# Kernel optimization log

Hardware: AMD Instinct MI355X
Metric: run time of the kernel (lower is better)

## Reference

```python
import jax, jax.numpy as jnp
import numpy as np

WINDOW_SIZE = 11
SIGMA = 1.5
C1 = 0.01 ** 2
C2 = 0.03 ** 2


def _make_window(channel, dtype=jnp.float32):
    # Faithful to torch `gaussian`: center at window_size/2 (= 5.5 for ws=11)
    x = np.arange(WINDOW_SIZE, dtype=np.float64)
    g = np.exp(-((x - WINDOW_SIZE / 2) ** 2) / (2.0 * SIGMA ** 2))
    g = (g / g.sum()).astype(np.float32)
    w2d = np.outer(g, g)  # (ws, ws)
    w = np.broadcast_to(w2d, (channel, 1, WINDOW_SIZE, WINDOW_SIZE)).copy()
    return jnp.asarray(w, dtype=dtype)


def _dwconv(x, w, channel):
    pad = WINDOW_SIZE // 2
    return jax.lax.conv_general_dilated(
        x, w,
        window_strides=(1, 1),
        padding=[(pad, pad), (pad, pad)],
        dimension_numbers=("NCHW", "OIHW", "NCHW"),
        feature_group_count=channel,
    )


def setup_inputs() -> dict:
    key = jax.random.key(0)
    k1, k2 = jax.random.split(key)
    B, C, H, W = 16, 3, 512, 512
    img1 = jax.random.uniform(k1, (B, C, H, W), dtype=jnp.float32)
    img2 = jax.random.uniform(k2, (B, C, H, W), dtype=jnp.float32)
    return {"img1": img1, "img2": img2}


def reference(img1, img2):
    channel = img1.shape[1]
    window = _make_window(channel, img1.dtype)

    mu1 = _dwconv(img1, window, channel)
    mu2 = _dwconv(img2, window, channel)
    mu1_sq = mu1 * mu1
    mu2_sq = mu2 * mu2
    mu1_mu2 = mu1 * mu2

    sigma1_sq = _dwconv(img1 * img1, window, channel) - mu1_sq
    sigma2_sq = _dwconv(img2 * img2, window, channel) - mu2_sq
    sigma12 = _dwconv(img1 * img2, window, channel) - mu1_mu2

    numerator = (2 * mu1_mu2 + C1) * (2 * sigma12 + C2)
    denominator = (mu1_sq + mu2_sq + C1) * (sigma1_sq + sigma2_sq + C2)
    ssim_map = numerator / denominator
    return jnp.mean(ssim_map)  # size_average=True
```

## Files before the change

kernel.cpp:

```cpp
#include <hip/hip_runtime.h>
#include <cmath>


#define IMG_H 512
#define IMG_W 512
#define STRIPE 32
#define NSTR (IMG_H / STRIPE)
#define NPLANES 48
#define NBLOCKS (NPLANES * NSTR)
#define SSIM_C1 (0.01f * 0.01f)
#define SSIM_C2 (0.03f * 0.03f)

struct W11 { float w[11]; };

__launch_bounds__(512, 2)
__global__ void ssim_main(const float* __restrict__ img1,
                          const float* __restrict__ img2,
                          float* __restrict__ blockSums, W11 wv) {
    __shared__ float2 tb[2][528];
    __shared__ float red[8];

    const int x = threadIdx.x;
    const int bid = blockIdx.x;
    const int plane = bid >> 4;
    const int stripe = bid & (NSTR - 1);
    const int y0 = stripe * STRIPE;
    const size_t base = (size_t)plane * (IMG_H * IMG_W);

    if (x < 10) {
        const int col = (x < 5) ? x : (x + 512);
        tb[0][col] = make_float2(0.f, 0.f);
        tb[1][col] = make_float2(0.f, 0.f);
    }

    float rA[11], rB[11], rS[11], rP[11];
    float acc = 0.f;

    float pa = 0.f, pb = 0.f;
    {
        const int r0 = y0 - 5;
        if (r0 >= 0) {
            pa = img1[base + (size_t)r0 * IMG_W + x];
            pb = img2[base + (size_t)r0 * IMG_W + x];
        }
    }

    int buf = 0;
#pragma unroll 1
    for (int c = 0; c < 4; ++c) {
#pragma unroll
        for (int j = 0; j < 11; ++j) {
            const int i = c * 11 + j;
            if (i < 42) {
                tb[buf][x + 5] = make_float2(pa, pb);
                pa = 0.f; pb = 0.f;
                const int rn = y0 - 4 + i;
                if (i + 1 < 42 && rn >= 0 && rn < IMG_H) {
                    pa = img1[base + (size_t)rn * IMG_W + x];
                    pb = img2[base + (size_t)rn * IMG_W + x];
                }
                __syncthreads();
                float h0 = 0.f, h1 = 0.f, h2 = 0.f, h3 = 0.f;
#pragma unroll
                for (int k = 0; k < 11; ++k) {
                    const float2 t = tb[buf][x + k];
                    const float w = wv.w[k];
                    const float sq = fmaf(t.y, t.y, t.x * t.x);
                    const float pr = t.x * t.y;
                    h0 = fmaf(w, t.x, h0);
                    h1 = fmaf(w, t.y, h1);
                    h2 = fmaf(w, sq, h2);
                    h3 = fmaf(w, pr, h3);
                }
                rA[j] = h0; rB[j] = h1; rS[j] = h2; rP[j] = h3;

                if (i >= 10) {
                    float vA = 0.f, vB = 0.f, vS = 0.f, vP = 0.f;
#pragma unroll
                    for (int k = 0; k < 11; ++k) {
                        const int s = (j + 1 + k) % 11;
                        const float w = wv.w[k];
                        vA = fmaf(w, rA[s], vA);
                        vB = fmaf(w, rB[s], vB);
                        vS = fmaf(w, rS[s], vS);
                        vP = fmaf(w, rP[s], vP);
                    }
                    const float mu11 = vA * vA;
                    const float mu22 = vB * vB;
                    const float mu12 = vA * vB;
                    const float num = fmaf(2.f, mu12, SSIM_C1) *
                                      fmaf(2.f, vP - mu12, SSIM_C2);
                    const float d1  = mu11 + mu22;
                    const float den = (d1 + SSIM_C1) * ((vS - d1) + SSIM_C2);
                    acc = fmaf(num, __builtin_amdgcn_rcpf(den), acc);
                }
                buf ^= 1;
            }
        }
    }

#pragma unroll
    for (int off = 32; off >= 1; off >>= 1)
        acc += __shfl_down(acc, off, 64);
    const int wave = x >> 6, lane = x & 63;
    if (lane == 0) red[wave] = acc;
    __syncthreads();
    if (x == 0) {
        float s = 0.f;
#pragma unroll
        for (int k = 0; k < 8; ++k) s += red[k];
        blockSums[bid] = s;
    }
}

__global__ void ssim_reduce(const float* __restrict__ bs,
                            float* __restrict__ out) {
    __shared__ double red[4];
    const int t = threadIdx.x;
    double a = 0.0;
    for (int idx = t; idx < NBLOCKS; idx += 256) a += (double)bs[idx];
#pragma unroll
    for (int off = 32; off >= 1; off >>= 1)
        a += __shfl_down(a, off, 64);
    const int wave = t >> 6, lane = t & 63;
    if (lane == 0) red[wave] = a;
    __syncthreads();
    if (t == 0) {
        const double s = red[0] + red[1] + red[2] + red[3];
        out[0] = (float)(s / (double)((double)NPLANES * IMG_H * IMG_W));
    }
}

extern "C" void kernel_launch(void* const* d_in, const int* in_sizes, int n_in,
                              void* d_out, int out_size, void* d_ws, size_t ws_size,
                              hipStream_t stream) {
    const float* img1 = (const float*)d_in[0];
    const float* img2 = (const float*)d_in[1];
    float* out = (float*)d_out;
    float* bs = (float*)d_ws;

    W11 wv;
    double g[11], s = 0.0;
    for (int i = 0; i < 11; ++i) {
        const double d = (double)i - 5.5;
        g[i] = exp(-(d * d) / (2.0 * 1.5 * 1.5));
        s += g[i];
    }
    for (int i = 0; i < 11; ++i) wv.w[i] = (float)(g[i] / s);

    ssim_main<<<NBLOCKS, 512, 0, stream>>>(img1, img2, bs, wv);
    ssim_reduce<<<1, 256, 0, stream>>>(bs, out);
}
```

Measured before the change: 150.8 us.

## Compute two output columns per thread with vectorized loads and 256-thread blocks

Each thread now handles two adjacent columns. Global loads become float2, and shared-memory reads become float4, so a 12-wide window is loaded once and reused for both columns' horizontal sums. The block size halves to 256 threads and the launch bounds change to 256,3. This cuts shared-memory traffic and instruction overhead per output pixel, but it doubles the per-thread register arrays (8x11 floats), which risks spills or lower occupancy.

Result: no change. 153.3 us (+1.6%).

```diff
diff --git a/kernel.cpp b/kernel.cpp
--- a/kernel.cpp
+++ b/kernel.cpp
@@ -13,35 +13,36 @@
 
 struct W11 { float w[11]; };
 
-__launch_bounds__(512, 2)
+__launch_bounds__(256, 3)
 __global__ void ssim_main(const float* __restrict__ img1,
                           const float* __restrict__ img2,
                           float* __restrict__ blockSums, W11 wv) {
-    __shared__ float2 tb[2][528];
-    __shared__ float red[8];
+    __shared__ __align__(16) float2 tb[2][528];
+    __shared__ float red[4];
 
-    const int x = threadIdx.x;
+    const int t = threadIdx.x;
     const int bid = blockIdx.x;
     const int plane = bid >> 4;
     const int stripe = bid & (NSTR - 1);
     const int y0 = stripe * STRIPE;
     const size_t base = (size_t)plane * (IMG_H * IMG_W);
 
-    if (x < 10) {
-        const int col = (x < 5) ? x : (x + 512);
+    if (t < 10) {
+        const int col = (t < 5) ? t : (t + 512);
         tb[0][col] = make_float2(0.f, 0.f);
         tb[1][col] = make_float2(0.f, 0.f);
     }
 
-    float rA[11], rB[11], rS[11], rP[11];
+    float rA0[11], rB0[11], rS0[11], rP0[11];
+    float rA1[11], rB1[11], rS1[11], rP1[11];
     float acc = 0.f;
 
-    float pa = 0.f, pb = 0.f;
+    float2 pa = make_float2(0.f, 0.f), pb = make_float2(0.f, 0.f);
     {
         const int r0 = y0 - 5;
         if (r0 >= 0) {
-            pa = img1[base + (size_t)r0 * IMG_W + x];
-            pb = img2[base + (size_t)r0 * IMG_W + x];
+            pa = *(const float2*)(img1 + base + (size_t)r0 * IMG_W + 2 * t);
+            pb = *(const float2*)(img2 + base + (size_t)r0 * IMG_W + 2 * t);
         }
     }
 
@@ -52,47 +53,84 @@
         for (int j = 0; j < 11; ++j) {
             const int i = c * 11 + j;
             if (i < 42) {
-                tb[buf][x + 5] = make_float2(pa, pb);
-                pa = 0.f; pb = 0.f;
+                tb[buf][2 * t + 5] = make_float2(pa.x, pb.x);
+                tb[buf][2 * t + 6] = make_float2(pa.y, pb.y);
+                pa = make_float2(0.f, 0.f); pb = make_float2(0.f, 0.f);
                 const int rn = y0 - 4 + i;
                 if (i + 1 < 42 && rn >= 0 && rn < IMG_H) {
-                    pa = img1[base + (size_t)rn * IMG_W + x];
-                    pb = img2[base + (size_t)rn * IMG_W + x];
+                    pa = *(const float2*)(img1 + base + (size_t)rn * IMG_W + 2 * t);
+                    pb = *(const float2*)(img2 + base + (size_t)rn * IMG_W + 2 * t);
                 }
                 __syncthreads();
-                float h0 = 0.f, h1 = 0.f, h2 = 0.f, h3 = 0.f;
+
+                float ta[12], tbv[12];
 #pragma unroll
-                for (int k = 0; k < 11; ++k) {
-                    const float2 t = tb[buf][x + k];
-                    const float w = wv.w[k];
-                    const float sq = fmaf(t.y, t.y, t.x * t.x);
-                    const float pr = t.x * t.y;
-                    h0 = fmaf(w, t.x, h0);
-                    h1 = fmaf(w, t.y, h1);
-                    h2 = fmaf(w, sq, h2);
-                    h3 = fmaf(w, pr, h3);
+                for (int k = 0; k < 6; ++k) {
+                    const float4 q = *(const float4*)(&tb[buf][2 * t + 2 * k]);
+                    ta[2 * k]     = q.x; tbv[2 * k]     = q.y;
+                    ta[2 * k + 1] = q.z; tbv[2 * k + 1] = q.w;
                 }
-                rA[j] = h0; rB[j] = h1; rS[j] = h2; rP[j] = h3;
+                float hA0 = 0.f, hB0 = 0.f, hS0 = 0.f, hP0 = 0.f;
+                float hA1 = 0.f, hB1 = 0.f, hS1 = 0.f, hP1 = 0.f;
+#pragma unroll
+                for (int m = 0; m < 12; ++m) {
+                    const float a = ta[m], b = tbv[m];
+                    const float sq = fmaf(b, b, a * a);
+                    const float pr = a * b;
+                    if (m <= 10) {
+                        const float w = wv.w[m];
+                        hA0 = fmaf(w, a, hA0);
+                        hB0 = fmaf(w, b, hB0);
+                        hS0 = fmaf(w, sq, hS0);
+                        hP0 = fmaf(w, pr, hP0);
+                    }
+                    if (m >= 1) {
+                        const float w = wv.w[m - 1];
+                        hA1 = fmaf(w, a, hA1);
+                        hB1 = fmaf(w, b, hB1);
+                        hS1 = fmaf(w, sq, hS1);
+                        hP1 = fmaf(w, pr, hP1);
+                    }
+                }
+                rA0[j] = hA0; rB0[j] = hB0; rS0[j] = hS0; rP0[j] = hP0;
+                rA1[j] = hA1; rB1[j] = hB1; rS1[j] = hS1; rP1[j] = hP1;
 
                 if (i >= 10) {
-                    float vA = 0.f, vB = 0.f, vS = 0.f, vP = 0.f;
+                    float vA0 = 0.f, vB0 = 0.f, vS0 = 0.f, vP0 = 0.f;
+                    float vA1 = 0.f, vB1 = 0.f, vS1 = 0.f, vP1 = 0.f;
 #pragma unroll
                     for (int k = 0; k < 11; ++k) {
                         const int s = (j + 1 + k) % 11;
                         const float w = wv.w[k];
-                        vA = fmaf(w, rA[s], vA);
-                        vB = fmaf(w, rB[s], vB);
-                        vS = fmaf(w, rS[s], vS);
-                        vP = fmaf(w, rP[s], vP);
+                        vA0 = fmaf(w, rA0[s], vA0);
+                        vB0 = fmaf(w, rB0[s], vB0);
+                        vS0 = fmaf(w, rS0[s], vS0);
+                        vP0 = fmaf(w, rP0[s], vP0);
+                        vA1 = fmaf(w, rA1[s], vA1);
+                        vB1 = fmaf(w, rB1[s], vB1);
+                        vS1 = fmaf(w, rS1[s], vS1);
+                        vP1 = fmaf(w, rP1[s], vP1);
                     }
-                    const float mu11 = vA * vA;
-                    const float mu22 = vB * vB;
-                    const float mu12 = vA * vB;
-                    const float num = fmaf(2.f, mu12, SSIM_C1) *
-                                      fmaf(2.f, vP - mu12, SSIM_C2);
-                    const float d1  = mu11 + mu22;
-                    const float den = (d1 + SSIM_C1) * ((vS - d1) + SSIM_C2);
-                    acc = fmaf(num, __builtin_amdgcn_rcpf(den), acc);
+                    {
+                        const float mu11 = vA0 * vA0;
+                        const float mu22 = vB0 * vB0;
+                        const float mu12 = vA0 * vB0;
+                        const float num = fmaf(2.f, mu12, SSIM_C1) *
+                                          fmaf(2.f, vP0 - mu12, SSIM_C2);
+                        const float d1  = mu11 + mu22;
+                        const float den = (d1 + SSIM_C1) * ((vS0 - d1) + SSIM_C2);
+                        acc = fmaf(num, __builtin_amdgcn_rcpf(den), acc);
+                    }
+                    {
+                        const float mu11 = vA1 * vA1;
+                        const float mu22 = vB1 * vB1;
+                        const float mu12 = vA1 * vB1;
+                        const float num = fmaf(2.f, mu12, SSIM_C1) *
+                                          fmaf(2.f, vP1 - mu12, SSIM_C2);
+                        const float d1  = mu11 + mu22;
+                        const float den = (d1 + SSIM_C1) * ((vS1 - d1) + SSIM_C2);
+                        acc = fmaf(num, __builtin_amdgcn_rcpf(den), acc);
+                    }
                 }
                 buf ^= 1;
             }
@@ -102,15 +140,10 @@
 #pragma unroll
     for (int off = 32; off >= 1; off >>= 1)
         acc += __shfl_down(acc, off, 64);
-    const int wave = x >> 6, lane = x & 63;
+    const int wave = t >> 6, lane = t & 63;
     if (lane == 0) red[wave] = acc;
     __syncthreads();
-    if (x == 0) {
-        float s = 0.f;
-#pragma unroll
-        for (int k = 0; k < 8; ++k) s += red[k];
-        blockSums[bid] = s;
-    }
+    if (t == 0) blockSums[bid] = red[0] + red[1] + red[2] + red[3];
 }
 
 __global__ void ssim_reduce(const float* __restrict__ bs,
@@ -148,6 +181,6 @@
     }
     for (int i = 0; i < 11; ++i) wv.w[i] = (float)(g[i] / s);
 
-    ssim_main<<<NBLOCKS, 512, 0, stream>>>(img1, img2, bs, wv);
+    ssim_main<<<NBLOCKS, 256, 0, stream>>>(img1, img2, bs, wv);
     ssim_reduce<<<1, 256, 0, stream>>>(bs, out);
 }
```
